# Kernel tuning notes

Measured on AMD Instinct MI355X. Metric: run time of the kernel, lower is better.

## Reference

```python
import jax, jax.numpy as jnp
import numpy as np
import math

THETA = 10000.0

def _rope(x, pos):
    # x: [B, H, S, Dh], pos: [S]
    d = x.shape[-1]
    inv_freq = 1.0 / (THETA ** (jnp.arange(0, d, 2, dtype=jnp.float32) / d))  # [Dh/2]
    ang = pos.astype(jnp.float32)[:, None] * inv_freq[None, :]                # [S, Dh/2]
    cos, sin = jnp.cos(ang), jnp.sin(ang)
    x1, x2 = x[..., 0::2], x[..., 1::2]
    r1 = x1 * cos - x2 * sin
    r2 = x1 * sin + x2 * cos
    return jnp.stack([r1, r2], axis=-1).reshape(x.shape)

def setup_inputs() -> dict:
    key = jax.random.key(0)
    ks = jax.random.split(key, 5)
    B, S, D = 2, 1024, 2048
    Dkv = 512
    scale = 1.0 / math.sqrt(D)
    return {
        "X": jax.random.normal(ks[0], (B, S, D), dtype=jnp.float32),
        "token_positions": jnp.arange(S, dtype=jnp.int32),
        "q_w": jax.random.normal(ks[1], (D, D), dtype=jnp.float32) * scale,
        "k_w": jax.random.normal(ks[2], (Dkv, D), dtype=jnp.float32) * scale,
        "v_w": jax.random.normal(ks[3], (Dkv, D), dtype=jnp.float32) * scale,
        "o_w": jax.random.normal(ks[4], (D, D), dtype=jnp.float32) * scale,
    }

def reference(X, token_positions, q_w, k_w, v_w, o_w):
    B, S, D = X.shape
    H, Hkv = 32, 8
    Dh = D // H
    G = H // Hkv  # query heads per KV head

    Q = (X @ q_w.T).reshape(B, S, H, Dh).transpose(0, 2, 1, 3)      # [B,H,S,Dh]
    K = (X @ k_w.T).reshape(B, S, Hkv, Dh).transpose(0, 2, 1, 3)    # [B,Hkv,S,Dh]
    V = (X @ v_w.T).reshape(B, S, Hkv, Dh).transpose(0, 2, 1, 3)    # [B,Hkv,S,Dh]

    Q = _rope(Q, token_positions)
    K = _rope(K, token_positions)

    # group query heads: [B, Hkv, G, S, Dh]
    Qg = Q.reshape(B, Hkv, G, S, Dh)
    scores = jnp.einsum('bkgqd,bkld->bkgql', Qg, K) / math.sqrt(Dh)  # [B,Hkv,G,S,S]
    causal = jnp.tril(jnp.ones((S, S), dtype=bool))
    scores = jnp.where(causal, scores, -jnp.inf)
    probs = jax.nn.softmax(scores, axis=-1)
    attn = jnp.einsum('bkgql,bkld->bkgqd', probs, V)                 # [B,Hkv,G,S,Dh]

    attn = attn.reshape(B, H, S, Dh).transpose(0, 2, 1, 3).reshape(B, S, D)
    return attn @ o_w.T
```

## Files before the change

### kernel.cpp

```cpp
#include <hip/hip_runtime.h>

typedef _Float16 f16;
typedef _Float16 half8 __attribute__((ext_vector_type(8), may_alias));
typedef _Float16 half4 __attribute__((ext_vector_type(4), may_alias));
typedef float f32x4 __attribute__((ext_vector_type(4), may_alias));

#define ROPE_KF -0.41524101186092027f

__device__ __forceinline__ void gload_lds16(const f16* g, f16* lds) {
  __builtin_amdgcn_global_load_lds(
      (const __attribute__((address_space(1))) void*)g,
      (__attribute__((address_space(3))) void*)lds, 16, 0, 0);
}

__device__ __forceinline__ half8 rope8(half8 v, float posf, int i0, float scale) {
  half8 r;
#pragma unroll
  for (int p = 0; p < 4; ++p) {
    const float ang = posf * exp2f(ROPE_KF * (float)(i0 + p));
    float s, c;
    sincosf(ang, &s, &c);
    const float x1 = (float)v[2 * p], x2 = (float)v[2 * p + 1];
    r[2 * p]     = (f16)((x1 * c - x2 * s) * scale);
    r[2 * p + 1] = (f16)((x1 * s + x2 * c) * scale);
  }
  return r;
}

__global__ __launch_bounds__(256) void cvt_all(const float* __restrict__ s0, f16* __restrict__ d0, int n0,
                                               const float* __restrict__ s1, f16* __restrict__ d1, int n1,
                                               const float* __restrict__ s2, f16* __restrict__ d2, int n2,
                                               const float* __restrict__ s3, f16* __restrict__ d3, int n3,
                                               const float* __restrict__ s4, f16* __restrict__ d4, int n4) {
  const int step = gridDim.x * blockDim.x * 4;
  const int base = (blockIdx.x * blockDim.x + threadIdx.x) * 4;
  auto go = [&](const float* s, f16* d, int n) {
    for (int i = base; i < n; i += step) {
      float4 v = *(const float4*)(s + i);
      half4 h;
      h[0] = (f16)v.x; h[1] = (f16)v.y; h[2] = (f16)v.z; h[3] = (f16)v.w;
      *(half4*)(d + i) = h;
    }
  };
  go(s0, d0, n0); go(s1, d1, n1); go(s2, d2, n2); go(s3, d3, n3); go(s4, d4, n4);
}

template <int OUT_F32>
__global__ __launch_bounds__(256) void gemm_bt(const f16* __restrict__ A,
                                               const f16* __restrict__ B,
                                               void* __restrict__ Cv,
                                               int M, int N, int K) {
  __shared__ alignas(16) f16 As[2][64][32];
  __shared__ alignas(16) f16 Bs[2][128][32];
  const int tid = threadIdx.x;
  const int w = tid >> 6, l = tid & 63;
  const int m0 = blockIdx.y << 6, n0 = blockIdx.x << 7;
  const int fr = l & 15;
  const int fkz = (((l >> 4) ^ ((fr >> 1) & 3)) << 3);
  const int srow = l >> 2;
  const int scol = (((l & 3) ^ ((l >> 3) & 3)) << 3);

  const f16* ga  = A + (size_t)(m0 + w * 16 + srow) * K + scol;
  const f16* gb0 = B + (size_t)(n0 + w * 16 + srow) * K + scol;
  const f16* gb1 = B + (size_t)(n0 + 64 + w * 16 + srow) * K + scol;

  auto stage = [&](int buf, int k0) {
    gload_lds16(ga + k0, &As[buf][w * 16][0]);
    gload_lds16(gb0 + k0, &Bs[buf][w * 16][0]);
    gload_lds16(gb1 + k0, &Bs[buf][64 + w * 16][0]);
  };

  f32x4 acc[4][2] = {};

  stage(0, 0);
  __syncthreads();
  const int nk = K >> 5;
  for (int t = 0; t < nk; ++t) {
    const int buf = t & 1;
    if (t + 1 < nk) stage(buf ^ 1, (t + 1) << 5);
    half8 af[4], bf[2];
#pragma unroll
    for (int i = 0; i < 4; ++i) af[i] = *(const half8*)&As[buf][i * 16 + fr][fkz];
#pragma unroll
    for (int j = 0; j < 2; ++j) bf[j] = *(const half8*)&Bs[buf][w * 32 + j * 16 + fr][fkz];
#pragma unroll
    for (int i = 0; i < 4; ++i)
#pragma unroll
      for (int j = 0; j < 2; ++j)
        acc[i][j] = __builtin_amdgcn_mfma_f32_16x16x32_f16(af[i], bf[j], acc[i][j], 0, 0, 0);
    __syncthreads();
  }

  const int orow = (l >> 4) << 2;
#pragma unroll
  for (int i = 0; i < 4; ++i) {
#pragma unroll
    for (int j = 0; j < 2; ++j) {
      const int col = n0 + w * 32 + j * 16 + fr;
#pragma unroll
      for (int r = 0; r < 4; ++r) {
        const size_t idx = (size_t)(m0 + i * 16 + orow + r) * N + col;
        if (OUT_F32) ((float*)Cv)[idx] = acc[i][j][r];
        else ((f16*)Cv)[idx] = (f16)acc[i][j][r];
      }
    }
  }
}

__global__ __launch_bounds__(256) void attn_fwd(const f16* __restrict__ QKV,
                                                const int* __restrict__ pos,
                                                f16* __restrict__ O) {
  const int flat = blockIdx.x + (blockIdx.y << 3) + (blockIdx.z << 8);
  const int rmid = ((flat & 7) << 6) + (flat >> 3);
  const int pr = rmid & 7, h = (rmid >> 3) & 31, b = rmid >> 8;
  const int kvh = h >> 2;
  const int tid = threadIdx.x, w = tid >> 6, l = tid & 63;
  const int fr = l & 15, g = l >> 4;
  const int orow = g << 2;
  const int qtA = pr, qtB = 15 - pr;

  __shared__ alignas(16) char KsB[8192];
  __shared__ alignas(16) char VtB[8192];
  __shared__ alignas(16) f16 Ps[4][16][72];

  auto KS = [&](int row, int slot) -> f16* {
    return (f16*)(KsB + row * 128 + ((slot ^ (row & 7)) << 4));
  };
  auto VT = [&](int d, int oct) -> f16* {
    return (f16*)(VtB + d * 128 + ((oct ^ (d & 7)) << 4));
  };

  const int sA = qtA * 64 + w * 16 + fr, sB = qtB * 64 + w * 16 + fr;
  const float pA = (float)pos[sA], pB = (float)pos[sB];
  const size_t qoff = (size_t)(b * 1024 + w * 16 + fr) * 3072 + h * 64 + (g << 3);
  const f16* qA = QKV + qoff + (size_t)qtA * 64 * 3072;
  const f16* qB = QKV + qoff + (size_t)qtB * 64 * 3072;
  const half8 aA0 = rope8(*(const half8*)qA, pA, g << 2, 0.125f);
  const half8 aA1 = rope8(*(const half8*)(qA + 32), pA, 16 + (g << 2), 0.125f);
  const half8 aB0 = rope8(*(const half8*)qB, pB, g << 2, 0.125f);
  const half8 aB1 = rope8(*(const half8*)(qB + 32), pB, 16 + (g << 2), 0.125f);

  float rmA[4], rlA[4], rmB[4], rlB[4];
  f32x4 oA[4] = {}, oB[4] = {};
#pragma unroll
  for (int r = 0; r < 4; ++r) { rmA[r] = rmB[r] = -3.0e38f; rlA[r] = rlB[r] = 0.f; }

  const int srow = tid >> 3, sds = tid & 7;
  const int vd = tid & 63, voct0 = tid >> 6;

  const f16* Kbase = QKV + 2048 + kvh * 64;
  const f16* Vbase = QKV + 2560 + kvh * 64;

  auto compute = [&](const half8& a0, const half8& a1, float* rm, float* rl,
                     f32x4* o, int qt, int kt) {
    f32x4 s4[4] = {};
#pragma unroll
    for (int j = 0; j < 4; ++j) {
      const half8 bk0 = *(const half8*)KS(j * 16 + fr, g);
      const half8 bk1 = *(const half8*)KS(j * 16 + fr, 4 + g);
      s4[j] = __builtin_amdgcn_mfma_f32_16x16x32_f16(a0, bk0, s4[j], 0, 0, 0);
      s4[j] = __builtin_amdgcn_mfma_f32_16x16x32_f16(a1, bk1, s4[j], 0, 0, 0);
    }
    if (kt == qt) {
      const int qrow0 = qt * 64 + w * 16 + orow;
#pragma unroll
      for (int j = 0; j < 4; ++j) {
        const int col = kt * 64 + j * 16 + fr;
#pragma unroll
        for (int r = 0; r < 4; ++r)
          if (col > qrow0 + r) s4[j][r] = -1.0e30f;
      }
    }
#pragma unroll
    for (int r = 0; r < 4; ++r) {
      float mx = fmaxf(fmaxf(s4[0][r], s4[1][r]), fmaxf(s4[2][r], s4[3][r]));
#pragma unroll
      for (int off = 8; off >= 1; off >>= 1) mx = fmaxf(mx, __shfl_xor(mx, off));
      const float mn = fmaxf(rm[r], mx);
      const float sf = __expf(rm[r] - mn);
      rl[r] *= sf;
      o[0][r] *= sf; o[1][r] *= sf; o[2][r] *= sf; o[3][r] *= sf;
      rm[r] = mn;
    }
    float ps[4] = {0.f, 0.f, 0.f, 0.f};
#pragma unroll
    for (int j = 0; j < 4; ++j)
#pragma unroll
      for (int r = 0; r < 4; ++r) {
        const float p = __expf(s4[j][r] - rm[r]);
        ps[r] += p;
        Ps[w][orow + r][j * 16 + fr] = (f16)p;
      }
#pragma unroll
    for (int r = 0; r < 4; ++r) {
      float t = ps[r];
#pragma unroll
      for (int off = 8; off >= 1; off >>= 1) t += __shfl_xor(t, off);
      rl[r] += t;
    }
#pragma unroll
    for (int kv2 = 0; kv2 < 2; ++kv2) {
      const half8 ap = *(const half8*)&Ps[w][fr][kv2 * 32 + (g << 3)];
#pragma unroll
      for (int j = 0; j < 4; ++j) {
        const half8 bv = *(const half8*)VT(j * 16 + fr, kv2 * 4 + g);
        o[j] = __builtin_amdgcn_mfma_f32_16x16x32_f16(ap, bv, o[j], 0, 0, 0);
      }
    }
  };

  for (int kt = 0; kt <= qtB; ++kt) {
    const int kvr = b * 1024 + (kt << 6);
#pragma unroll
    for (int p = 0; p < 2; ++p) {
      const int row = srow + (p << 5);
      half8 kk = *(const half8*)(Kbase + (size_t)(kvr + row) * 3072 + sds * 8);
      kk = rope8(kk, (float)pos[(kt << 6) + row], sds << 2, 1.0f);
      *(half8*)KS(row, sds) = kk;
    }
#pragma unroll
    for (int it = 0; it < 2; ++it) {
      const int oct = voct0 + (it << 2);
      const f16* gv = Vbase + (size_t)(kvr + oct * 8) * 3072 + vd;
      half8 vv;
#pragma unroll
      for (int m = 0; m < 8; ++m) vv[m] = gv[(size_t)m * 3072];
      *(half8*)VT(vd, oct) = vv;
    }
    __syncthreads();
    if (kt <= qtA) compute(aA0, aA1, rmA, rlA, oA, qtA, kt);
    compute(aB0, aB1, rmB, rlB, oB, qtB, kt);
    __syncthreads();
  }

#pragma unroll
  for (int j = 0; j < 4; ++j)
#pragma unroll
    for (int r = 0; r < 4; ++r) {
      const int rowA = qtA * 64 + w * 16 + orow + r;
      const int rowB = qtB * 64 + w * 16 + orow + r;
      const int col = h * 64 + j * 16 + fr;
      O[(size_t)(b * 1024 + rowA) * 2048 + col] = (f16)(oA[j][r] / rlA[r]);
      O[(size_t)(b * 1024 + rowB) * 2048 + col] = (f16)(oB[j][r] / rlB[r]);
    }
}

extern "C" void kernel_launch(void* const* d_in, const int* in_sizes, int n_in,
                              void* d_out, int out_size, void* d_ws, size_t ws_size,
                              hipStream_t stream) {
  const float* X = (const float*)d_in[0];
  const int* tokpos = (const int*)d_in[1];
  const float* qw = (const float*)d_in[2];
  const float* kw = (const float*)d_in[3];
  const float* vw = (const float*)d_in[4];
  const float* ow = (const float*)d_in[5];

  constexpr int B = 2, S = 1024, D = 2048, DKV = 512, H = 32;
  constexpr int M = B * S;
  constexpr int NQKV = D + 2 * DKV;

  char* ws = (char*)d_ws;
  f16* Xh   = (f16*)(ws);
  f16* QKVW = (f16*)(ws + (8u << 20));
  f16* owh  = (f16*)(ws + (20u << 20));
  f16* QKVc = (f16*)(ws + (28u << 20));
  f16* Ah   = (f16*)(ws + (40u << 20));

  cvt_all<<<2048, 256, 0, stream>>>(X, Xh, M * D,
                                    qw, QKVW, D * D,
                                    kw, QKVW + (size_t)D * D, DKV * D,
                                    vw, QKVW + (size_t)(D + DKV) * D, DKV * D,
                                    ow, owh, D * D);

  gemm_bt<0><<<dim3(NQKV / 128, M / 64), 256, 0, stream>>>(Xh, QKVW, QKVc, M, NQKV, D);

  attn_fwd<<<dim3(8, H, B), 256, 0, stream>>>(QKVc, tokpos, Ah);

  gemm_bt<1><<<dim3(D / 128, M / 64), 256, 0, stream>>>(Ah, owh, d_out, M, D, D);
}
```

Before: 151.1 us.

## Pre-repack roped K and transposed V, double-buffer attention tiles via async LDS loads

Adds a repack kernel that applies RoPE to K once and writes K and transposed V as pre-swizzled contiguous 64x64 tiles into workspace. The attention kernel then streams these tiles straight into double-buffered LDS with global_load_lds, prefetching the next tile while computing the current one. This removes the per-block redundant RoPE on K (each K tile was recomputed by every query-head block), the strided scalar V transpose loads, and one barrier per iteration. In exchange it adds an extra kernel launch and global round trip, and doubles LDS use. Kp/Vt reuse the Xh workspace region, which is safe only because Xh is no longer read after the QKV GEMM.

```diff
diff --git a/kernel.cpp b/kernel.cpp
--- a/kernel.cpp
+++ b/kernel.cpp
@@ -107,7 +107,41 @@
   }
 }
 
+__global__ __launch_bounds__(256) void repack_kv(const f16* __restrict__ QKV,
+                                                 const int* __restrict__ pos,
+                                                 f16* __restrict__ Kp,
+                                                 f16* __restrict__ Vt) {
+  const int kt = blockIdx.x, kvh = blockIdx.y, b = blockIdx.z;
+  const int tid = threadIdx.x;
+  __shared__ f16 vs[64][72];
+  const size_t tile = ((size_t)((b * 8 + kvh) * 16 + kt)) * 4096;
+  const f16* kbase = QKV + 2048 + kvh * 64;
+  const f16* vbase = QKV + 2560 + kvh * 64;
+#pragma unroll
+  for (int p = 0; p < 2; ++p) {
+    const int c = tid + p * 256;
+    const int row = c >> 3, slot = c & 7;
+    const size_t grow = (size_t)(b * 1024 + kt * 64 + row) * 3072;
+    half8 kk = *(const half8*)(kbase + grow + slot * 8);
+    kk = rope8(kk, (float)pos[kt * 64 + row], slot << 2, 1.0f);
+    *(half8*)(Kp + tile + row * 64 + ((slot ^ (row & 7)) << 3)) = kk;
+    *(half8*)&vs[row][slot * 8] = *(const half8*)(vbase + grow + slot * 8);
+  }
+  __syncthreads();
+#pragma unroll
+  for (int p = 0; p < 2; ++p) {
+    const int c = tid + p * 256;
+    const int d = c >> 3, oct = c & 7;
+    half8 vv;
+#pragma unroll
+    for (int m = 0; m < 8; ++m) vv[m] = vs[oct * 8 + m][d];
+    *(half8*)(Vt + tile + d * 64 + ((oct ^ (d & 7)) << 3)) = vv;
+  }
+}
+
 __global__ __launch_bounds__(256) void attn_fwd(const f16* __restrict__ QKV,
+                                                const f16* __restrict__ Kp,
+                                                const f16* __restrict__ Vt,
                                                 const int* __restrict__ pos,
                                                 f16* __restrict__ O) {
   const int flat = blockIdx.x + (blockIdx.y << 3) + (blockIdx.z << 8);
@@ -119,15 +153,15 @@
   const int orow = g << 2;
   const int qtA = pr, qtB = 15 - pr;
 
-  __shared__ alignas(16) char KsB[8192];
-  __shared__ alignas(16) char VtB[8192];
+  __shared__ alignas(16) char KsB[2][8192];
+  __shared__ alignas(16) char VtB[2][8192];
   __shared__ alignas(16) f16 Ps[4][16][72];
 
-  auto KS = [&](int row, int slot) -> f16* {
-    return (f16*)(KsB + row * 128 + ((slot ^ (row & 7)) << 4));
-  };
-  auto VT = [&](int d, int oct) -> f16* {
-    return (f16*)(VtB + d * 128 + ((oct ^ (d & 7)) << 4));
+  auto KS = [&](int buf, int row, int slot) -> f16* {
+    return (f16*)(KsB[buf] + row * 128 + ((slot ^ (row & 7)) << 4));
+  };
+  auto VT = [&](int buf, int d, int oct) -> f16* {
+    return (f16*)(VtB[buf] + d * 128 + ((oct ^ (d & 7)) << 4));
   };
 
   const int sA = qtA * 64 + w * 16 + fr, sB = qtB * 64 + w * 16 + fr;
@@ -145,19 +179,27 @@
 #pragma unroll
   for (int r = 0; r < 4; ++r) { rmA[r] = rmB[r] = -3.0e38f; rlA[r] = rlB[r] = 0.f; }
 
-  const int srow = tid >> 3, sds = tid & 7;
-  const int vd = tid & 63, voct0 = tid >> 6;
-
-  const f16* Kbase = QKV + 2048 + kvh * 64;
-  const f16* Vbase = QKV + 2560 + kvh * 64;
-
-  auto compute = [&](const half8& a0, const half8& a1, float* rm, float* rl,
+  const size_t tbase = ((size_t)((b * 8 + kvh) * 16)) * 4096;
+  const f16* kp0 = Kp + tbase + w * 1024 + (l << 3);
+  const f16* vp0 = Vt + tbase + w * 1024 + (l << 3);
+  auto stage = [&](int buf, int kt) {
+    const f16* kp = kp0 + (size_t)kt * 4096;
+    const f16* vp = vp0 + (size_t)kt * 4096;
+    f16* kl = (f16*)(KsB[buf] + w * 2048);
+    f16* vl = (f16*)(VtB[buf] + w * 2048);
+    gload_lds16(kp, kl);
+    gload_lds16(kp + 512, kl + 512);
+    gload_lds16(vp, vl);
+    gload_lds16(vp + 512, vl + 512);
+  };
+
+  auto compute = [&](int buf, const half8& a0, const half8& a1, float* rm, float* rl,
                      f32x4* o, int qt, int kt) {
     f32x4 s4[4] = {};
 #pragma unroll
     for (int j = 0; j < 4; ++j) {
-      const half8 bk0 = *(const half8*)KS(j * 16 + fr, g);
-      const half8 bk1 = *(const half8*)KS(j * 16 + fr, 4 + g);
+      const half8 bk0 = *(const half8*)KS(buf, j * 16 + fr, g);
+      const half8 bk1 = *(const half8*)KS(buf, j * 16 + fr, 4 + g);
       s4[j] = __builtin_amdgcn_mfma_f32_16x16x32_f16(a0, bk0, s4[j], 0, 0, 0);
       s4[j] = __builtin_amdgcn_mfma_f32_16x16x32_f16(a1, bk1, s4[j], 0, 0, 0);
     }
@@ -203,33 +245,19 @@
       const half8 ap = *(const half8*)&Ps[w][fr][kv2 * 32 + (g << 3)];
 #pragma unroll
       for (int j = 0; j < 4; ++j) {
-        const half8 bv = *(const half8*)VT(j * 16 + fr, kv2 * 4 + g);
+        const half8 bv = *(const half8*)VT(buf, j * 16 + fr, kv2 * 4 + g);
         o[j] = __builtin_amdgcn_mfma_f32_16x16x32_f16(ap, bv, o[j], 0, 0, 0);
       }
     }
   };
 
+  stage(0, 0);
+  __syncthreads();
   for (int kt = 0; kt <= qtB; ++kt) {
-    const int kvr = b * 1024 + (kt << 6);
-#pragma unroll
-    for (int p = 0; p < 2; ++p) {
-      const int row = srow + (p << 5);
-      half8 kk = *(const half8*)(Kbase + (size_t)(kvr + row) * 3072 + sds * 8);
-      kk = rope8(kk, (float)pos[(kt << 6) + row], sds << 2, 1.0f);
-      *(half8*)KS(row, sds) = kk;
-    }
-#pragma unroll
-    for (int it = 0; it < 2; ++it) {
-      const int oct = voct0 + (it << 2);
-      const f16* gv = Vbase + (size_t)(kvr + oct * 8) * 3072 + vd;
-      half8 vv;
-#pragma unroll
-      for (int m = 0; m < 8; ++m) vv[m] = gv[(size_t)m * 3072];
-      *(half8*)VT(vd, oct) = vv;
-    }
-    __syncthreads();
-    if (kt <= qtA) compute(aA0, aA1, rmA, rlA, oA, qtA, kt);
-    compute(aB0, aB1, rmB, rlB, oB, qtB, kt);
+    const int buf = kt & 1;
+    if (kt < qtB) stage(buf ^ 1, kt + 1);
+    if (kt <= qtA) compute(buf, aA0, aA1, rmA, rlA, oA, qtA, kt);
+    compute(buf, aB0, aB1, rmB, rlB, oB, qtB, kt);
     __syncthreads();
   }
 
@@ -265,6 +293,8 @@
   f16* owh  = (f16*)(ws + (20u << 20));
   f16* QKVc = (f16*)(ws + (28u << 20));
   f16* Ah   = (f16*)(ws + (40u << 20));
+  f16* Kp   = (f16*)(ws);
+  f16* Vt   = (f16*)(ws + (2u << 20));
 
   cvt_all<<<2048, 256, 0, stream>>>(X, Xh, M * D,
                                     qw, QKVW, D * D,
@@ -274,7 +304,9 @@
 
   gemm_bt<0><<<dim3(NQKV / 128, M / 64), 256, 0, stream>>>(Xh, QKVW, QKVc, M, NQKV, D);
 
-  attn_fwd<<<dim3(8, H, B), 256, 0, stream>>>(QKVc, tokpos, Ah);
+  repack_kv<<<dim3(16, 8, 2), 256, 0, stream>>>(QKVc, tokpos, Kp, Vt);
+
+  attn_fwd<<<dim3(8, H, B), 256, 0, stream>>>(QKVc, Kp, Vt, tokpos, Ah);
 
   gemm_bt<1><<<dim3(D / 128, M / 64), 256, 0, stream>>>(Ah, owh, d_out, M, D, D);
 }
```

Result: faster. 140.2 us (-7.2%).
